# Optimization experiments

Measured on AMD Instinct MI355X. Metric: run time of the kernel, lower is better.

The kernel has to match this reference:

```python
import jax, jax.numpy as jnp
import numpy as np

D_MODEL = 1024
N_HEAD = 16
D_K = D_MODEL // N_HEAD


def setup_inputs() -> dict:
    key = jax.random.key(0)
    ks = jax.random.split(key, 12)
    B, S = 2, 2048
    s = 1.0 / np.sqrt(D_MODEL)
    return {
        "query": jax.random.normal(ks[0], (B, S, D_MODEL), jnp.float32),
        "key": jax.random.normal(ks[1], (B, S, D_MODEL), jnp.float32),
        "value": jax.random.normal(ks[2], (B, S, D_MODEL), jnp.float32),
        "Wq": jax.random.normal(ks[3], (D_MODEL, D_MODEL), jnp.float32) * s,
        "bq": jnp.zeros((D_MODEL,), jnp.float32),
        "Wk": jax.random.normal(ks[4], (D_MODEL, D_MODEL), jnp.float32) * s,
        "bk": jnp.zeros((D_MODEL,), jnp.float32),
        "Wv": jax.random.normal(ks[5], (D_MODEL, D_MODEL), jnp.float32) * s,
        "bv": jnp.zeros((D_MODEL,), jnp.float32),
        "Wo": jax.random.normal(ks[6], (D_MODEL, D_MODEL), jnp.float32) * s,
        "bo": jnp.zeros((D_MODEL,), jnp.float32),
    }


def reference(query, key, value, Wq, bq, Wk, bk, Wv, bv, Wo, bo):
    B, S, _ = query.shape
    # QKV projections (torch Linear: x @ W.T + b)
    q = query @ Wq.T + bq
    k = key @ Wk.T + bk
    v = value @ Wv.T + bv
    # [B, S, H, Dk] -> [B, H, S, Dk]
    q = q.reshape(B, S, N_HEAD, D_K).transpose(0, 2, 1, 3)
    k = k.reshape(B, -1, N_HEAD, D_K).transpose(0, 2, 1, 3)
    v = v.reshape(B, -1, N_HEAD, D_K).transpose(0, 2, 1, 3)
    # scores [B, H, Sq, Sk]
    attn = jnp.einsum("bhqd,bhkd->bhqk", q, k) / jnp.sqrt(jnp.float32(D_K))
    attn = jax.nn.softmax(attn, axis=-1)  # dropout p=0 -> identity
    out = jnp.einsum("bhqk,bhkd->bhqd", attn, v)
    out = out.transpose(0, 2, 1, 3).reshape(B, S, D_MODEL)
    return out @ Wo.T + bo
```

## Files before the change

kernel.cpp:

```cpp
#include <hip/hip_runtime.h>
#include <cstdint>
#include <cstddef>

#define DM 1024
#define NHEAD 16
#define DKH 64
#define SEQLEN 2048
#define NBATCH 2
#define MTOT (NBATCH * SEQLEN)

typedef __attribute__((ext_vector_type(8))) short bf16x8;
typedef __attribute__((ext_vector_type(4))) float f32x4;
typedef __attribute__((ext_vector_type(16))) float f32x16;
typedef __attribute__((ext_vector_type(2))) unsigned int u32x2;

#define QSCALE 0.18033688011112042f

__device__ __forceinline__ uint16_t f2bf(float f) {
  uint32_t x = __float_as_uint(f);
  uint32_t r = x + 0x7FFFu + ((x >> 16) & 1u);
  return (uint16_t)(r >> 16);
}

__device__ __forceinline__ uint32_t cvtpk(float a, float b) {
  uint32_t r;
  asm("v_cvt_pk_bf16_f32 %0, %1, %2" : "=v"(r) : "v"(a), "v"(b));
  return r;
}

__device__ __forceinline__ float exp2_fast(float x) {
  float r;
  asm("v_exp_f32 %0, %1" : "=v"(r) : "v"(x));
  return r;
}

__device__ __forceinline__ float max3f(float a, float b, float c) {
  float r;
  asm("v_max3_f32 %0, %1, %2, %3" : "=v"(r) : "v"(a), "v"(b), "v"(c));
  return r;
}

__device__ __forceinline__ void gload_lds16(const void* g, void* l) {
  __builtin_amdgcn_global_load_lds(
      (const __attribute__((address_space(1))) void*)g,
      (__attribute__((address_space(3))) void*)l, 16, 0, 0);
}

__device__ __forceinline__ int fsw(int r) { return ((r + (r >> 3)) & 7) << 4; }

struct CvtArgs {
  const float* src[7];
  uint16_t* dst[7];
  int end4[7];
};

__global__ void cvt_all_kernel(CvtArgs a) {
  int i = blockIdx.x * blockDim.x + threadIdx.x;
  int r = 0;
#pragma unroll
  for (int j = 0; j < 7; ++j)
    if (i >= a.end4[j]) r = j + 1;
  if (r >= 7) return;
  int local = i - (r == 0 ? 0 : a.end4[r - 1]);
  float4 v = reinterpret_cast<const float4*>(a.src[r])[local];
  uint64_t p = (uint64_t)f2bf(v.x) | ((uint64_t)f2bf(v.y) << 16) |
               ((uint64_t)f2bf(v.z) << 32) | ((uint64_t)f2bf(v.w) << 48);
  reinterpret_cast<uint64_t*>(a.dst[r])[local] = p;
}

__device__ __forceinline__ void gemm_stage(const uint16_t* __restrict__ A,
                                           const uint16_t* __restrict__ Bt,
                                           int brow, int bcol, int k0,
                                           char* smem, int buf, int wave, int lane) {
#pragma unroll
  for (int t = 0; t < 8; ++t) {
    const int o = t * 4096 + wave * 1024 + lane * 16;
    const uint16_t* g;
    if (t < 4) {
      const int row = o >> 7, kk = (o & 127) >> 1;
      g = A + (size_t)(brow + row) * DM + (k0 + kk);
    } else {
      const int o2 = o - 16384;
      const int row = o2 >> 7, kk = (o2 & 127) >> 1;
      g = Bt + (size_t)(bcol + row) * DM + (k0 + kk);
    }
    gload_lds16(g, smem + buf * 32768 + t * 4096 + wave * 1024);
  }
}

__global__ __launch_bounds__(256)
void gemm_qkv(const uint16_t* __restrict__ xq, const uint16_t* __restrict__ xk,
              const uint16_t* __restrict__ xv, const uint16_t* __restrict__ wqkv,
              const float* __restrict__ bqp, const float* __restrict__ bkp,
              const float* __restrict__ bvp, uint16_t* __restrict__ Qp,
              uint16_t* __restrict__ Kp, uint16_t* __restrict__ VTp) {
  __shared__ uint16_t smem[2 * 2 * 128 * 64];
  const int swz = (blockIdx.x & 7) * 96 + (blockIdx.x >> 3);
  const int bx = swz & 31, by = swz >> 5;
  const int tid = threadIdx.x;
  const int wave = tid >> 6, lane = tid & 63;
  const int l15 = lane & 15, l4 = lane >> 4;
  const int proj = by >> 3;
  const int brow = bx * 128, bcol = (by & 7) * 128;
  const int wr = (wave >> 1) * 64, wc = (wave & 1) * 64;
  const uint16_t* A = proj == 0 ? xq : proj == 1 ? xk : xv;
  const uint16_t* Bt = wqkv + (size_t)proj * DM * DM;
  const float* bias = proj == 0 ? bqp : proj == 1 ? bkp : bvp;

  const f32x4 fzero = {0.f, 0.f, 0.f, 0.f};
  f32x4 acc[4][4];
#pragma unroll
  for (int m = 0; m < 4; ++m)
#pragma unroll
    for (int n = 0; n < 4; ++n) acc[m][n] = fzero;

  gemm_stage(A, Bt, brow, bcol, 0, (char*)smem, 0, wave, lane);
  int cur = 0;
  for (int k0 = 0; k0 < DM; k0 += 64) {
    __syncthreads();
    if (k0 + 64 < DM)
      gemm_stage(A, Bt, brow, bcol, k0 + 64, (char*)smem, cur ^ 1, wave, lane);
    const uint16_t* At = smem + cur * 16384;
    const uint16_t* Bs = At + 8192;
#pragma unroll
    for (int ks = 0; ks < 2; ++ks) {
      bf16x8 a[4], b[4];
#pragma unroll
      for (int m = 0; m < 4; ++m)
        a[m] = *(const bf16x8*)(At + (wr + m * 16 + l15) * 64 + ks * 32 + l4 * 8);
#pragma unroll
      for (int n = 0; n < 4; ++n)
        b[n] = *(const bf16x8*)(Bs + (wc + n * 16 + l15) * 64 + ks * 32 + l4 * 8);
#pragma unroll
      for (int m = 0; m < 4; ++m)
#pragma unroll
        for (int n = 0; n < 4; ++n)
          acc[m][n] = __builtin_amdgcn_mfma_f32_16x16x32_bf16(a[m], b[n], acc[m][n], 0, 0, 0);
    }
    cur ^= 1;
  }

  const float scale = proj == 0 ? QSCALE : 1.0f;
  uint16_t* dstQK = proj == 0 ? Qp : Kp;
#pragma unroll
  for (int m = 0; m < 4; ++m) {
#pragma unroll
    for (int n = 0; n < 4; ++n) {
      const int gcol = bcol + wc + n * 16 + l15;
      const float bv = bias[gcol];
      if (proj == 2) {
        const int grow0 = brow + wr + m * 16 + l4 * 4;
        const int b_ = grow0 >> 11, s_ = grow0 & 2047;
        const int h_ = gcol >> 6, d_ = gcol & 63;
        uint16_t* dst = VTp + ((size_t)((b_ * NHEAD + h_) * DKH + d_)) * SEQLEN + s_;
        uint64_t pk = (uint64_t)f2bf(acc[m][n][0] + bv) |
                      ((uint64_t)f2bf(acc[m][n][1] + bv) << 16) |
                      ((uint64_t)f2bf(acc[m][n][2] + bv) << 32) |
                      ((uint64_t)f2bf(acc[m][n][3] + bv) << 48);
        *(uint64_t*)dst = pk;
      } else {
#pragma unroll
        for (int r = 0; r < 4; ++r) {
          const int grow = brow + wr + m * 16 + l4 * 4 + r;
          dstQK[(size_t)grow * DM + gcol] = f2bf((acc[m][n][r] + bv) * scale);
        }
      }
    }
  }
}

__global__ __launch_bounds__(256)
void gemm_out(const uint16_t* __restrict__ A, const uint16_t* __restrict__ Bt,
              const float* __restrict__ bias, float* __restrict__ C) {
  __shared__ uint16_t smem[2 * 2 * 128 * 64];
  const int swz = (blockIdx.x & 7) * 32 + (blockIdx.x >> 3);
  const int tid = threadIdx.x;
  const int wave = tid >> 6, lane = tid & 63;
  const int l15 = lane & 15, l4 = lane >> 4;
  const int brow = (swz & 31) * 128, bcol = (swz >> 5) * 128;
  const int wr = (wave >> 1) * 64, wc = (wave & 1) * 64;

  const f32x4 fzero = {0.f, 0.f, 0.f, 0.f};
  f32x4 acc[4][4];
#pragma unroll
  for (int m = 0; m < 4; ++m)
#pragma unroll
    for (int n = 0; n < 4; ++n) acc[m][n] = fzero;

  gemm_stage(A, Bt, brow, bcol, 0, (char*)smem, 0, wave, lane);
  int cur = 0;
  for (int k0 = 0; k0 < DM; k0 += 64) {
    __syncthreads();
    if (k0 + 64 < DM)
      gemm_stage(A, Bt, brow, bcol, k0 + 64, (char*)smem, cur ^ 1, wave, lane);
    const uint16_t* At = smem + cur * 16384;
    const uint16_t* Bs = At + 8192;
#pragma unroll
    for (int ks = 0; ks < 2; ++ks) {
      bf16x8 a[4], b[4];
#pragma unroll
      for (int m = 0; m < 4; ++m)
        a[m] = *(const bf16x8*)(At + (wr + m * 16 + l15) * 64 + ks * 32 + l4 * 8);
#pragma unroll
      for (int n = 0; n < 4; ++n)
        b[n] = *(const bf16x8*)(Bs + (wc + n * 16 + l15) * 64 + ks * 32 + l4 * 8);
#pragma unroll
      for (int m = 0; m < 4; ++m)
#pragma unroll
        for (int n = 0; n < 4; ++n)
          acc[m][n] = __builtin_amdgcn_mfma_f32_16x16x32_bf16(a[m], b[n], acc[m][n], 0, 0, 0);
    }
    cur ^= 1;
  }

#pragma unroll
  for (int m = 0; m < 4; ++m) {
#pragma unroll
    for (int n = 0; n < 4; ++n) {
      const int gcol = bcol + wc + n * 16 + l15;
      const float bv = bias[gcol];
#pragma unroll
      for (int r = 0; r < 4; ++r) {
        const int grow = brow + wr + m * 16 + l4 * 4 + r;
        C[(size_t)grow * DM + gcol] = acc[m][n][r] + bv;
      }
    }
  }
}

__device__ __forceinline__ void stage_kv(const uint16_t* __restrict__ Kg,
                                         const uint16_t* __restrict__ Vg,
                                         char* buf, int wave, int lane) {
#pragma unroll
  for (int i = 0; i < 2; ++i) {
    const int base = i * 4096 + wave * 1024;
    const int row = i * 32 + wave * 8 + (lane >> 3);
    const int esw = (((lane & 7) << 4) ^ fsw(row)) >> 1;
    gload_lds16(Kg + (size_t)row * DM + esw, buf + base);
    gload_lds16(Vg + (size_t)row * SEQLEN + esw, buf + 8192 + base);
  }
}

__global__ __launch_bounds__(256)
void attn_fwd_kernel(const uint16_t* __restrict__ Qp, const uint16_t* __restrict__ Kp,
                     const uint16_t* __restrict__ VTp, uint16_t* __restrict__ Op) {
  __shared__ __align__(16) char lds[32768];
  const int swz = (blockIdx.x & 7) * 64 + (blockIdx.x >> 3);
  const int bb = swz >> 8, h = (swz >> 4) & 15;
  const int q0 = (swz & 15) * 128;
  const int tid = threadIdx.x;
  const int wave = tid >> 6, lane = tid & 63;
  const int l31 = lane & 31, hi = lane >> 5;

  const int qrow = q0 + wave * 32 + l31;
  const uint16_t* qb = Qp + ((size_t)(bb * SEQLEN + qrow)) * DM + h * DKH;
  bf16x8 qf[4];
#pragma unroll
  for (int ds = 0; ds < 4; ++ds)
    qf[ds] = *(const bf16x8*)(qb + ds * 16 + hi * 8);

  bf16x8 onesf;
#pragma unroll
  for (int j = 0; j < 8; ++j) onesf[j] = (short)0x3F80;

  f32x16 oacc[2], lacc, zero16;
#pragma unroll
  for (int r = 0; r < 16; ++r) {
    oacc[0][r] = 0.f; oacc[1][r] = 0.f; lacc[r] = 0.f; zero16[r] = 0.f;
  }
  float mrow = -1e30f;

  const uint16_t* Kg = Kp + ((size_t)(bb * SEQLEN)) * DM + h * DKH;
  const uint16_t* Vg = VTp + ((size_t)((bb * NHEAD + h) * DKH)) * SEQLEN;

  stage_kv(Kg, Vg, lds, wave, lane);

  const int NT = SEQLEN / 64;
  for (int t = 0; t < NT; ++t) {
    __syncthreads();
    if (t + 1 < NT)
      stage_kv(Kg + (size_t)(t + 1) * 64 * DM, Vg + (t + 1) * 64,
               lds + ((t + 1) & 1) * 16384, wave, lane);
    const char* kb = lds + (t & 1) * 16384;
    const char* vb = kb + 8192;

    f32x16 sacc[2];
    __builtin_amdgcn_s_setprio(1);
#pragma unroll
    for (int n = 0; n < 2; ++n) {
      const int kr = 32 * n + l31;
      const char* krow = kb + kr * 128;
      const int f = fsw(kr);
      const bf16x8 kf0 = *(const bf16x8*)(krow + ((hi * 16) ^ f));
      sacc[n] = __builtin_amdgcn_mfma_f32_32x32x16_bf16(kf0, qf[0], zero16, 0, 0, 0);
#pragma unroll
      for (int ds = 1; ds < 4; ++ds) {
        const bf16x8 kf = *(const bf16x8*)(krow + ((ds * 32 + hi * 16) ^ f));
        sacc[n] = __builtin_amdgcn_mfma_f32_32x32x16_bf16(kf, qf[ds], sacc[n], 0, 0, 0);
      }
    }
    __builtin_amdgcn_s_setprio(0);

    float ma = max3f(sacc[0][0], sacc[0][1], sacc[0][2]);
    ma = max3f(ma, sacc[0][3], sacc[0][4]);
    ma = max3f(ma, sacc[0][5], sacc[0][6]);
    ma = max3f(ma, sacc[0][7], sacc[0][8]);
    ma = max3f(ma, sacc[0][9], sacc[0][10]);
    ma = max3f(ma, sacc[0][11], sacc[0][12]);
    ma = max3f(ma, sacc[0][13], sacc[0][14]);
    float mb = max3f(sacc[1][0], sacc[1][1], sacc[1][2]);
    mb = max3f(mb, sacc[1][3], sacc[1][4]);
    mb = max3f(mb, sacc[1][5], sacc[1][6]);
    mb = max3f(mb, sacc[1][7], sacc[1][8]);
    mb = max3f(mb, sacc[1][9], sacc[1][10]);
    mb = max3f(mb, sacc[1][11], sacc[1][12]);
    mb = max3f(mb, sacc[1][13], sacc[1][14]);
    float mx = max3f(fmaxf(ma, sacc[0][15]), mb, sacc[1][15]);
    mx = fmaxf(mx, __shfl_xor(mx, 32, 64));

    float mnew = mrow;
    if (__any(mx > mrow + 8.f)) {
      mnew = fmaxf(mrow, mx);
      const float scl = exp2_fast(mrow - mnew);
#pragma unroll
      for (int m = 0; m < 2; ++m)
#pragma unroll
        for (int r = 0; r < 16; ++r) oacc[m][r] *= scl;
      lacc[0] *= scl;
    }
    mrow = mnew;

#pragma unroll
    for (int n = 0; n < 2; ++n) {
      float pv[16];
#pragma unroll
      for (int r = 0; r < 16; ++r) pv[r] = exp2_fast(sacc[n][r] - mnew);
      const uint32_t c0 = cvtpk(pv[0], pv[1]),   c1 = cvtpk(pv[2], pv[3]);
      const uint32_t c2 = cvtpk(pv[4], pv[5]),   c3 = cvtpk(pv[6], pv[7]);
      const uint32_t c4 = cvtpk(pv[8], pv[9]),   c5 = cvtpk(pv[10], pv[11]);
      const uint32_t c6 = cvtpk(pv[12], pv[13]), c7 = cvtpk(pv[14], pv[15]);
      const u32x2 r02 = __builtin_amdgcn_permlane32_swap(c0, c2, false, false);
      const u32x2 r13 = __builtin_amdgcn_permlane32_swap(c1, c3, false, false);
      const u32x2 r46 = __builtin_amdgcn_permlane32_swap(c4, c6, false, false);
      const u32x2 r57 = __builtin_amdgcn_permlane32_swap(c5, c7, false, false);
      union { uint32_t w[4]; bf16x8 v; } f0, f1;
      f0.w[0] = r02.x; f0.w[1] = r13.x; f0.w[2] = r02.y; f0.w[3] = r13.y;
      f1.w[0] = r46.x; f1.w[1] = r57.x; f1.w[2] = r46.y; f1.w[3] = r57.y;

      __builtin_amdgcn_s_setprio(1);
#pragma unroll
      for (int m = 0; m < 2; ++m) {
        const int vr = 32 * m + l31;
        const char* vrow = vb + vr * 128;
        const int f = fsw(vr);
        const bf16x8 v0 = *(const bf16x8*)(vrow + ((n * 64 + hi * 16) ^ f));
        const bf16x8 v1 = *(const bf16x8*)(vrow + ((n * 64 + 32 + hi * 16) ^ f));
        oacc[m] = __builtin_amdgcn_mfma_f32_32x32x16_bf16(v0, f0.v, oacc[m], 0, 0, 0);
        oacc[m] = __builtin_amdgcn_mfma_f32_32x32x16_bf16(v1, f1.v, oacc[m], 0, 0, 0);
      }
      lacc = __builtin_amdgcn_mfma_f32_32x32x16_bf16(onesf, f0.v, lacc, 0, 0, 0);
      lacc = __builtin_amdgcn_mfma_f32_32x32x16_bf16(onesf, f1.v, lacc, 0, 0, 0);
      __builtin_amdgcn_s_setprio(0);
    }
  }

  const float il = 1.0f / lacc[0];
  uint16_t* ob = Op + ((size_t)(bb * SEQLEN + qrow)) * DM + h * DKH;
#pragma unroll
  for (int m = 0; m < 2; ++m)
#pragma unroll
    for (int rq = 0; rq < 4; ++rq) {
      const uint32_t w0 = cvtpk(oacc[m][4 * rq + 0] * il, oacc[m][4 * rq + 1] * il);
      const uint32_t w1 = cvtpk(oacc[m][4 * rq + 2] * il, oacc[m][4 * rq + 3] * il);
      *(uint64_t*)(ob + 32 * m + 8 * rq + 4 * hi) =
          (uint64_t)w0 | ((uint64_t)w1 << 32);
    }
}

extern "C" void kernel_launch(void* const* d_in, const int* in_sizes, int n_in,
                              void* d_out, int out_size, void* d_ws, size_t ws_size,
                              hipStream_t stream) {
  (void)in_sizes; (void)n_in; (void)out_size; (void)ws_size;
  const float* query = (const float*)d_in[0];
  const float* key_i = (const float*)d_in[1];
  const float* value = (const float*)d_in[2];
  const float* Wq = (const float*)d_in[3];
  const float* bq = (const float*)d_in[4];
  const float* Wk = (const float*)d_in[5];
  const float* bk = (const float*)d_in[6];
  const float* Wv = (const float*)d_in[7];
  const float* bv = (const float*)d_in[8];
  const float* Wo = (const float*)d_in[9];
  const float* bo = (const float*)d_in[10];
  float* out = (float*)d_out;

  char* ws = (char*)d_ws;
  const size_t MB = 1ull << 20;
  uint16_t* xq  = (uint16_t*)(ws + 0 * MB);
  uint16_t* xk  = (uint16_t*)(ws + 8 * MB);
  uint16_t* xv  = (uint16_t*)(ws + 16 * MB);
  uint16_t* wqkv = (uint16_t*)(ws + 24 * MB);
  uint16_t* wob = (uint16_t*)(ws + 30 * MB);
  uint16_t* Qp  = (uint16_t*)(ws + 32 * MB);
  uint16_t* Kp  = (uint16_t*)(ws + 40 * MB);
  uint16_t* VTp = (uint16_t*)(ws + 48 * MB);
  uint16_t* AO  = (uint16_t*)(ws + 56 * MB);

  const int n4x = (MTOT * DM) / 4;
  const int n4w = (DM * DM) / 4;
  CvtArgs ca;
  ca.src[0] = query; ca.dst[0] = xq;
  ca.src[1] = key_i; ca.dst[1] = xk;
  ca.src[2] = value; ca.dst[2] = xv;
  ca.src[3] = Wq;    ca.dst[3] = wqkv;
  ca.src[4] = Wk;    ca.dst[4] = wqkv + DM * DM;
  ca.src[5] = Wv;    ca.dst[5] = wqkv + 2 * DM * DM;
  ca.src[6] = Wo;    ca.dst[6] = wob;
  int acc = 0;
  for (int j = 0; j < 7; ++j) { acc += (j < 3) ? n4x : n4w; ca.end4[j] = acc; }
  const int blk = 256;
  cvt_all_kernel<<<(acc + blk - 1) / blk, blk, 0, stream>>>(ca);

  gemm_qkv<<<768, 256, 0, stream>>>(xq, xk, xv, wqkv, bq, bk, bv, Qp, Kp, VTp);

  attn_fwd_kernel<<<512, 256, 0, stream>>>(Qp, Kp, VTp, AO);

  gemm_out<<<256, 256, 0, stream>>>(AO, wob, bo, out);
}
```

Before: 136.6 us.

## Split attention KV sequence across two wave groups and merge softmax partials

```diff
diff --git a/kernel.cpp b/kernel.cpp
--- a/kernel.cpp
+++ b/kernel.cpp
@@ -95,13 +95,11 @@
               const float* __restrict__ bvp, uint16_t* __restrict__ Qp,
               uint16_t* __restrict__ Kp, uint16_t* __restrict__ VTp) {
   __shared__ uint16_t smem[2 * 2 * 128 * 64];
-  const int swz = (blockIdx.x & 7) * 96 + (blockIdx.x >> 3);
-  const int bx = swz & 31, by = swz >> 5;
   const int tid = threadIdx.x;
   const int wave = tid >> 6, lane = tid & 63;
   const int l15 = lane & 15, l4 = lane >> 4;
-  const int proj = by >> 3;
-  const int brow = bx * 128, bcol = (by & 7) * 128;
+  const int proj = blockIdx.y >> 3;
+  const int brow = blockIdx.x * 128, bcol = (blockIdx.y & 7) * 128;
   const int wr = (wave >> 1) * 64, wc = (wave & 1) * 64;
   const uint16_t* A = proj == 0 ? xq : proj == 1 ? xk : xv;
   const uint16_t* Bt = wqkv + (size_t)proj * DM * DM;
@@ -173,11 +171,10 @@
 void gemm_out(const uint16_t* __restrict__ A, const uint16_t* __restrict__ Bt,
               const float* __restrict__ bias, float* __restrict__ C) {
   __shared__ uint16_t smem[2 * 2 * 128 * 64];
-  const int swz = (blockIdx.x & 7) * 32 + (blockIdx.x >> 3);
   const int tid = threadIdx.x;
   const int wave = tid >> 6, lane = tid & 63;
   const int l15 = lane & 15, l4 = lane >> 4;
-  const int brow = (swz & 31) * 128, bcol = (swz >> 5) * 128;
+  const int brow = blockIdx.x * 128, bcol = blockIdx.y * 128;
   const int wr = (wave >> 1) * 64, wc = (wave & 1) * 64;
 
   const f32x4 fzero = {0.f, 0.f, 0.f, 0.f};
@@ -230,29 +227,30 @@
 
 __device__ __forceinline__ void stage_kv(const uint16_t* __restrict__ Kg,
                                          const uint16_t* __restrict__ Vg,
-                                         char* buf, int wave, int lane) {
+                                         char* buf, int wq, int lane) {
 #pragma unroll
   for (int i = 0; i < 2; ++i) {
-    const int base = i * 4096 + wave * 1024;
-    const int row = i * 32 + wave * 8 + (lane >> 3);
+    const int base = i * 4096 + wq * 1024;
+    const int row = i * 32 + wq * 8 + (lane >> 3);
     const int esw = (((lane & 7) << 4) ^ fsw(row)) >> 1;
     gload_lds16(Kg + (size_t)row * DM + esw, buf + base);
     gload_lds16(Vg + (size_t)row * SEQLEN + esw, buf + 8192 + base);
   }
 }
 
-__global__ __launch_bounds__(256)
+__global__ __launch_bounds__(512)
 void attn_fwd_kernel(const uint16_t* __restrict__ Qp, const uint16_t* __restrict__ Kp,
                      const uint16_t* __restrict__ VTp, uint16_t* __restrict__ Op) {
-  __shared__ __align__(16) char lds[32768];
+  __shared__ __align__(16) char lds[65536];
   const int swz = (blockIdx.x & 7) * 64 + (blockIdx.x >> 3);
   const int bb = swz >> 8, h = (swz >> 4) & 15;
   const int q0 = (swz & 15) * 128;
   const int tid = threadIdx.x;
   const int wave = tid >> 6, lane = tid & 63;
+  const int wq = wave & 3, kh = wave >> 2;
   const int l31 = lane & 31, hi = lane >> 5;
 
-  const int qrow = q0 + wave * 32 + l31;
+  const int qrow = q0 + wq * 32 + l31;
   const uint16_t* qb = Qp + ((size_t)(bb * SEQLEN + qrow)) * DM + h * DKH;
   bf16x8 qf[4];
 #pragma unroll
@@ -270,18 +268,19 @@
   }
   float mrow = -1e30f;
 
-  const uint16_t* Kg = Kp + ((size_t)(bb * SEQLEN)) * DM + h * DKH;
-  const uint16_t* Vg = VTp + ((size_t)((bb * NHEAD + h) * DKH)) * SEQLEN;
-
-  stage_kv(Kg, Vg, lds, wave, lane);
-
-  const int NT = SEQLEN / 64;
+  const uint16_t* Kg = Kp + ((size_t)(bb * SEQLEN + kh * 1024)) * DM + h * DKH;
+  const uint16_t* Vg = VTp + ((size_t)((bb * NHEAD + h) * DKH)) * SEQLEN + kh * 1024;
+  char* my = lds + kh * 32768;
+
+  stage_kv(Kg, Vg, my, wq, lane);
+
+  const int NT = 1024 / 64;
   for (int t = 0; t < NT; ++t) {
     __syncthreads();
     if (t + 1 < NT)
       stage_kv(Kg + (size_t)(t + 1) * 64 * DM, Vg + (t + 1) * 64,
-               lds + ((t + 1) & 1) * 16384, wave, lane);
-    const char* kb = lds + (t & 1) * 16384;
+               my + ((t + 1) & 1) * 16384, wq, lane);
+    const char* kb = my + (t & 1) * 16384;
     const char* vb = kb + 8192;
 
     f32x16 sacc[2];
@@ -364,17 +363,41 @@
     }
   }
 
-  const float il = 1.0f / lacc[0];
+  __syncthreads();
+  char* mbuf = lds + wq * 16384 + lane * 144;
+  if (kh == 1) {
+    *(f32x16*)(mbuf) = oacc[0];
+    *(f32x16*)(mbuf + 64) = oacc[1];
+    *(float*)(mbuf + 128) = mrow;
+    *(float*)(mbuf + 132) = lacc[0];
+  }
+  __syncthreads();
+  if (kh == 1) return;
+
+  const f32x16 o2a = *(const f32x16*)(mbuf);
+  const f32x16 o2b = *(const f32x16*)(mbuf + 64);
+  const float m2 = *(const float*)(mbuf + 128);
+  const float l2 = *(const float*)(mbuf + 132);
+  const float mstar = fmaxf(mrow, m2);
+  const float a1 = exp2_fast(mrow - mstar);
+  const float a2 = exp2_fast(m2 - mstar);
+  const float il = 1.0f / (a1 * lacc[0] + a2 * l2);
+  const float w1 = a1 * il, w2 = a2 * il;
+
   uint16_t* ob = Op + ((size_t)(bb * SEQLEN + qrow)) * DM + h * DKH;
 #pragma unroll
-  for (int m = 0; m < 2; ++m)
+  for (int m = 0; m < 2; ++m) {
+    const f32x16 o2 = (m == 0) ? o2a : o2b;
 #pragma unroll
     for (int rq = 0; rq < 4; ++rq) {
-      const uint32_t w0 = cvtpk(oacc[m][4 * rq + 0] * il, oacc[m][4 * rq + 1] * il);
-      const uint32_t w1 = cvtpk(oacc[m][4 * rq + 2] * il, oacc[m][4 * rq + 3] * il);
+      const uint32_t w0 = cvtpk(oacc[m][4 * rq + 0] * w1 + o2[4 * rq + 0] * w2,
+                                oacc[m][4 * rq + 1] * w1 + o2[4 * rq + 1] * w2);
+      const uint32_t wA = cvtpk(oacc[m][4 * rq + 2] * w1 + o2[4 * rq + 2] * w2,
+                                oacc[m][4 * rq + 3] * w1 + o2[4 * rq + 3] * w2);
       *(uint64_t*)(ob + 32 * m + 8 * rq + 4 * hi) =
-          (uint64_t)w0 | ((uint64_t)w1 << 32);
-    }
+          (uint64_t)w0 | ((uint64_t)wA << 32);
+    }
+  }
 }
 
 extern "C" void kernel_launch(void* const* d_in, const int* in_sizes, int n_in,
@@ -421,9 +444,11 @@
   const int blk = 256;
   cvt_all_kernel<<<(acc + blk - 1) / blk, blk, 0, stream>>>(ca);
 
-  gemm_qkv<<<768, 256, 0, stream>>>(xq, xk, xv, wqkv, bq, bk, bv, Qp, Kp, VTp);
-
-  attn_fwd_kernel<<<512, 256, 0, stream>>>(Qp, Kp, VTp, AO);
-
-  gemm_out<<<256, 256, 0, stream>>>(AO, wob, bo, out);
-}
+  dim3 gq(MTOT / 128, 24);
+  gemm_qkv<<<gq, 256, 0, stream>>>(xq, xk, xv, wqkv, bq, bk, bv, Qp, Kp, VTp);
+
+  attn_fwd_kernel<<<512, 512, 0, stream>>>(Qp, Kp, VTp, AO);
+
+  dim3 gg(MTOT / 128, DM / 128);
+  gemm_out<<<gg, 256, 0, stream>>>(AO, wob, bo, out);
+}
```

Result: faster. 126.7 us (-7.2%).
